# Performance work log

Measured on AMD Instinct MI355X. Metric: run time of the kernel, lower is better.

Reference implementation:

```python
import jax, jax.numpy as jnp
import numpy as np

N_SPARSE = 2  # keep N of every M weights (2:4 structured sparsity)
M_SPARSE = 4


def compute_mask(w, n, m):
    # w: [out, in]; zero the (m - n) smallest-|w| entries in each group of m
    out_f, in_f = w.shape
    k = m - n
    wr = jnp.abs(w).reshape(out_f, in_f // m, m)
    # indices of the k smallest |w| per group (torch.topk largest=False)
    _, idx = jax.lax.top_k(-wr, k)                      # [out, in/m, k]
    pruned = jax.nn.one_hot(idx, m, dtype=w.dtype).sum(axis=-2)  # [out, in/m, m]
    mask = 1.0 - pruned
    return mask.reshape(out_f, in_f)


def setup_inputs() -> dict:
    key = jax.random.key(0)
    k1, k2, k3 = jax.random.split(key, 3)
    B, S, Din, Dout = 64, 197, 768, 3072
    x = jax.random.normal(k1, (B, S, Din), dtype=jnp.float32)
    weight = jax.random.normal(k2, (Dout, Din), dtype=jnp.float32)
    bias = jax.random.normal(k3, (Dout,), dtype=jnp.float32)
    return {"x": x, "weight": weight, "bias": bias}


def reference(x, weight, bias):
    # mask is a precomputed buffer in torch (not differentiated)
    mask = compute_mask(jax.lax.stop_gradient(weight), N_SPARSE, M_SPARSE)
    w = weight * mask
    # F.linear: x @ w.T + b
    return jnp.einsum('bsi,oi->bso', x, w) + bias
```

## Files before the change

kernel.cpp:

```cpp
#include <hip/hip_runtime.h>
#include <hip/hip_bf16.h>

#define M_DIM 12608
#define K_DIM 768
#define N_DIM 3072
#define M_PAD 12800
#define BM 256
#define BN 128
#define BK 32

typedef __attribute__((ext_vector_type(8))) short bf16x8;
typedef __attribute__((ext_vector_type(4))) float f32x4;

__device__ __forceinline__ void gload_lds16(const void* g, void* l) {
  __builtin_amdgcn_global_load_lds(
      (const __attribute__((address_space(1))) unsigned int*)g,
      (__attribute__((address_space(3))) unsigned int*)l,
      16, 0, 0);
}

#define GX 4800
#define GW 2304
__global__ void cvt_fused(const float* __restrict__ x, const float* __restrict__ w,
                          __hip_bfloat16* __restrict__ xb, __hip_bfloat16* __restrict__ wb) {
  if (blockIdx.x < GX) {
    size_t i = ((size_t)blockIdx.x * 256 + threadIdx.x) * 8;
    union { __hip_bfloat16 h[8]; uint4 u; } o;
    if (i < (size_t)M_DIM * K_DIM) {
      float4 a = *(const float4*)(x + i);
      float4 b = *(const float4*)(x + i + 4);
      o.h[0] = __float2bfloat16(a.x); o.h[1] = __float2bfloat16(a.y);
      o.h[2] = __float2bfloat16(a.z); o.h[3] = __float2bfloat16(a.w);
      o.h[4] = __float2bfloat16(b.x); o.h[5] = __float2bfloat16(b.y);
      o.h[6] = __float2bfloat16(b.z); o.h[7] = __float2bfloat16(b.w);
    } else {
      o.u = make_uint4(0, 0, 0, 0);
    }
    *(uint4*)(xb + i) = o.u;
  } else {
    size_t g = ((size_t)(blockIdx.x - GX) * 256 + threadIdx.x);
    float4 v = *(const float4*)(w + g * 4);
    float val[4] = {v.x, v.y, v.z, v.w};
    float a[4] = {fabsf(v.x), fabsf(v.y), fabsf(v.z), fabsf(v.w)};
    union { __hip_bfloat16 h[4]; uint2 u; } o;
#pragma unroll
    for (int i = 0; i < 4; ++i) {
      int rank = 0;
#pragma unroll
      for (int j = 0; j < 4; ++j)
        rank += (a[j] > a[i]) || (a[j] == a[i] && j > i);
      o.h[i] = __float2bfloat16(rank < 2 ? val[i] : 0.0f);
    }
    *(uint2*)(wb + g * 4) = o.u;
  }
}

__global__ __launch_bounds__(256, 2) void gemm_bt(
    const __hip_bfloat16* __restrict__ A,
    const __hip_bfloat16* __restrict__ B,
    const float* __restrict__ bias,
    float* __restrict__ C)
{
  __shared__ char smem[49152];

  const int tid  = threadIdx.x;
  const int lane = tid & 63;
  const int wave = tid >> 6;

  const int tile_m = blockIdx.y * BM;
  const int tile_n = blockIdx.x * BN;

  const int ris  = lane >> 2;
  const int slot = lane & 3;
  const __hip_bfloat16* agp[4];
  const __hip_bfloat16* bgp[2];
#pragma unroll
  for (int i = 0; i < 4; ++i) {
    const int arow = wave * 64 + i * 16 + ris;
    const int acg = slot ^ (arow & 3) ^ ((arow >> 2) & 3);
    agp[i] = A + (size_t)(tile_m + arow) * K_DIM + acg * 8;
  }
#pragma unroll
  for (int i = 0; i < 2; ++i) {
    const int brow = wave * 32 + i * 16 + ris;
    const int bcg = slot ^ (brow & 3) ^ ((brow >> 2) & 3);
    bgp[i] = B + (size_t)(tile_n + brow) * K_DIM + bcg * 8;
  }

  const int frow  = lane & 15;
  const int fslot = (lane >> 4) ^ (frow & 3) ^ ((frow >> 2) & 3);

  f32x4 acc[4][8] = {};

#pragma unroll
  for (int i = 0; i < 4; ++i)
    gload_lds16(agp[i], smem + (wave * 4 + i) * 1024);
#pragma unroll
  for (int i = 0; i < 2; ++i)
    gload_lds16(bgp[i], smem + 16384 + (wave * 2 + i) * 1024);

  const int NITER = K_DIM / BK;
#pragma unroll 2
  for (int k = 0; k < NITER; ++k) {
    const int cur = k & 1;
    __syncthreads();

    if (k + 1 < NITER) {
      const int off = (k + 1) * BK;
      char* bb = smem + (cur ^ 1) * 24576;
#pragma unroll
      for (int i = 0; i < 4; ++i)
        gload_lds16(agp[i] + off, bb + (wave * 4 + i) * 1024);
#pragma unroll
      for (int i = 0; i < 2; ++i)
        gload_lds16(bgp[i] + off, bb + 16384 + (wave * 2 + i) * 1024);
    }

    const char* sa = smem + cur * 24576;
    bf16x8 af[4], bfr[8];
#pragma unroll
    for (int i = 0; i < 4; ++i)
      af[i] = *(const bf16x8*)(sa + (wave * 64 + i * 16 + frow) * 64 + fslot * 16);
#pragma unroll
    for (int j = 0; j < 8; ++j)
      bfr[j] = *(const bf16x8*)(sa + 16384 + (j * 16 + frow) * 64 + fslot * 16);
#pragma unroll
    for (int i = 0; i < 4; ++i)
#pragma unroll
      for (int j = 0; j < 8; ++j)
        acc[i][j] = __builtin_amdgcn_mfma_f32_16x16x32_bf16(af[i], bfr[j], acc[i][j], 0, 0, 0);
  }

  const int ccol = lane & 15;
  const int quad = lane >> 4;
  float bv[8];
#pragma unroll
  for (int j = 0; j < 8; ++j)
    bv[j] = bias[tile_n + j * 16 + ccol];

  float* tr = (float*)smem + wave * 2112;
  const int erow = lane >> 2;
  const int eseg = lane & 3;

#pragma unroll
  for (int i = 0; i < 4; ++i) {
    __syncthreads();
#pragma unroll
    for (int j = 0; j < 8; ++j)
#pragma unroll
      for (int r = 0; r < 4; ++r)
        tr[(quad * 4 + r) * 132 + j * 16 + ccol] = acc[i][j][r] + bv[j];
    __syncthreads();
    const int grow = tile_m + wave * 64 + i * 16 + erow;
    if (grow < M_DIM) {
      float* dst = C + (size_t)grow * N_DIM + tile_n + eseg * 32;
      const float* src = tr + erow * 132 + eseg * 32;
#pragma unroll
      for (int u = 0; u < 8; ++u)
        *(f32x4*)(dst + u * 4) = *(const f32x4*)(src + u * 4);
    }
  }
}

extern "C" void kernel_launch(void* const* d_in, const int* in_sizes, int n_in,
                              void* d_out, int out_size, void* d_ws, size_t ws_size,
                              hipStream_t stream) {
  const float* x    = (const float*)d_in[0];
  const float* w    = (const float*)d_in[1];
  const float* bias = (const float*)d_in[2];
  float* out = (float*)d_out;

  __hip_bfloat16* xb = (__hip_bfloat16*)d_ws;
  __hip_bfloat16* wb = xb + (size_t)M_PAD * K_DIM;

  cvt_fused<<<GX + GW, 256, 0, stream>>>(x, w, xb, wb);

  dim3 grid(N_DIM / BN, M_PAD / BM);
  gemm_bt<<<grid, 256, 0, stream>>>(xb, wb, bias, out);
}
```

Measured before the change: 269.1 us.

## Restructure GEMM to 256x256 tiles with 8 waves and 4-stage LDS pipeline

Replaces the 256x128, 4-wave GEMM with a 256x256 tile run by 8 waves arranged 2x4. It uses a 4-deep LDS ring of 32 KB stages held in 128 KB of dynamic shared memory and issues loads two tiles ahead with explicit vmcnt waits and raw barriers. Each K-step is split into two MFMA phases raised with s_setprio, and blocks are remapped through an XCD-aware swizzle. The goal is more reuse per loaded byte and better overlap of loads with compute, at the cost of higher register and LDS pressure, which may limit occupancy to one block per CU.

```diff
diff --git a/kernel.cpp b/kernel.cpp
--- a/kernel.cpp
+++ b/kernel.cpp
@@ -6,8 +6,12 @@
 #define N_DIM 3072
 #define M_PAD 12800
 #define BM 256
-#define BN 128
+#define BN 256
 #define BK 32
+#define NT (K_DIM / BK)
+#define MBLK (M_PAD / BM)
+#define NBLK_N (N_DIM / BN)
+#define NWG (MBLK * NBLK_N)
 
 typedef __attribute__((ext_vector_type(8))) short bf16x8;
 typedef __attribute__((ext_vector_type(4))) float f32x4;
@@ -55,109 +59,134 @@
   }
 }
 
-__global__ __launch_bounds__(256, 2) void gemm_bt(
+__global__ __launch_bounds__(512, 2) void gemm_8p(
     const __hip_bfloat16* __restrict__ A,
     const __hip_bfloat16* __restrict__ B,
     const float* __restrict__ bias,
     float* __restrict__ C)
 {
-  __shared__ char smem[49152];
+  extern __shared__ char smem[];
 
   const int tid  = threadIdx.x;
   const int lane = tid & 63;
   const int wave = tid >> 6;
-
-  const int tile_m = blockIdx.y * BM;
-  const int tile_n = blockIdx.x * BN;
-
-  const int ris  = lane >> 2;
-  const int slot = lane & 3;
-  const __hip_bfloat16* agp[4];
-  const __hip_bfloat16* bgp[2];
-#pragma unroll
-  for (int i = 0; i < 4; ++i) {
-    const int arow = wave * 64 + i * 16 + ris;
-    const int acg = slot ^ (arow & 3) ^ ((arow >> 2) & 3);
-    agp[i] = A + (size_t)(tile_m + arow) * K_DIM + acg * 8;
-  }
-#pragma unroll
-  for (int i = 0; i < 2; ++i) {
-    const int brow = wave * 32 + i * 16 + ris;
-    const int bcg = slot ^ (brow & 3) ^ ((brow >> 2) & 3);
-    bgp[i] = B + (size_t)(tile_n + brow) * K_DIM + bcg * 8;
+  const int wm   = wave >> 2;
+  const int wn   = wave & 3;
+
+  const int wg  = blockIdx.x;
+  const int swz = (wg & 7) * (NWG / 8) + (wg >> 3);
+  const int tile_m = (swz / NBLK_N) * BM;
+  const int tile_n = (swz % NBLK_N) * BN;
+
+  const int r2 = lane >> 2;
+  const int p  = lane & 3;
+  const int fxor = (r2 & 3) ^ ((r2 >> 2) & 3);
+  const int gsw  = p ^ fxor;
+  const __hip_bfloat16* asrc[2];
+  const __hip_bfloat16* bsrc[2];
+#pragma unroll
+  for (int u = 0; u < 2; ++u) {
+    const int row = u * 128 + wave * 16 + r2;
+    asrc[u] = A + (size_t)(tile_m + row) * K_DIM + gsw * 8;
+    bsrc[u] = B + (size_t)(tile_n + row) * K_DIM + gsw * 8;
   }
 
   const int frow  = lane & 15;
   const int fslot = (lane >> 4) ^ (frow & 3) ^ ((frow >> 2) & 3);
-
-  f32x4 acc[4][8] = {};
-
-#pragma unroll
-  for (int i = 0; i < 4; ++i)
-    gload_lds16(agp[i], smem + (wave * 4 + i) * 1024);
-#pragma unroll
-  for (int i = 0; i < 2; ++i)
-    gload_lds16(bgp[i], smem + 16384 + (wave * 2 + i) * 1024);
-
-  const int NITER = K_DIM / BK;
-#pragma unroll 2
-  for (int k = 0; k < NITER; ++k) {
-    const int cur = k & 1;
-    __syncthreads();
-
-    if (k + 1 < NITER) {
-      const int off = (k + 1) * BK;
-      char* bb = smem + (cur ^ 1) * 24576;
-#pragma unroll
-      for (int i = 0; i < 4; ++i)
-        gload_lds16(agp[i] + off, bb + (wave * 4 + i) * 1024);
-#pragma unroll
-      for (int i = 0; i < 2; ++i)
-        gload_lds16(bgp[i] + off, bb + 16384 + (wave * 2 + i) * 1024);
-    }
-
-    const char* sa = smem + cur * 24576;
-    bf16x8 af[4], bfr[8];
-#pragma unroll
-    for (int i = 0; i < 4; ++i)
-      af[i] = *(const bf16x8*)(sa + (wave * 64 + i * 16 + frow) * 64 + fslot * 16);
-#pragma unroll
-    for (int j = 0; j < 8; ++j)
-      bfr[j] = *(const bf16x8*)(sa + 16384 + (j * 16 + frow) * 64 + fslot * 16);
-#pragma unroll
-    for (int i = 0; i < 4; ++i)
-#pragma unroll
-      for (int j = 0; j < 8; ++j)
-        acc[i][j] = __builtin_amdgcn_mfma_f32_16x16x32_bf16(af[i], bfr[j], acc[i][j], 0, 0, 0);
+  const int abase = (wm * 128 + frow) * 64 + fslot * 16;
+  const int bbase = 16384 + (wn * 64 + frow) * 64 + fslot * 16;
+
+  f32x4 acc[8][4] = {};
+
+#pragma unroll
+  for (int u = 0; u < 2; ++u)
+    gload_lds16(asrc[u], smem + u * 8192 + wave * 1024);
+#pragma unroll
+  for (int u = 0; u < 2; ++u)
+    gload_lds16(bsrc[u], smem + 16384 + u * 8192 + wave * 1024);
+#pragma unroll
+  for (int u = 0; u < 2; ++u)
+    gload_lds16(asrc[u] + BK, smem + 32768 + u * 8192 + wave * 1024);
+#pragma unroll
+  for (int u = 0; u < 2; ++u)
+    gload_lds16(bsrc[u] + BK, smem + 32768 + 16384 + u * 8192 + wave * 1024);
+  asm volatile("s_waitcnt vmcnt(4)" ::: "memory");
+  __builtin_amdgcn_s_barrier();
+
+#pragma unroll
+  for (int t = 0; t < NT; ++t) {
+    const int q  = t & 3;
+    const int qs = (t + 2) & 3;
+    const char* bq = smem + q * 32768;
+
+    bf16x8 af[4], bfv[4];
+#pragma unroll
+    for (int m = 0; m < 4; ++m)
+      af[m] = *(const bf16x8*)(bq + abase + m * 1024);
+#pragma unroll
+    for (int n = 0; n < 4; ++n)
+      bfv[n] = *(const bf16x8*)(bq + bbase + n * 1024);
+    if (t + 2 < NT) {
+#pragma unroll
+      for (int u = 0; u < 2; ++u)
+        gload_lds16(asrc[u] + (t + 2) * BK, smem + qs * 32768 + u * 8192 + wave * 1024);
+    }
+    __builtin_amdgcn_s_barrier();
+    __builtin_amdgcn_s_setprio(1);
+#pragma unroll
+    for (int m = 0; m < 4; ++m)
+#pragma unroll
+      for (int n = 0; n < 4; ++n)
+        acc[m][n] = __builtin_amdgcn_mfma_f32_16x16x32_bf16(af[m], bfv[n], acc[m][n], 0, 0, 0);
+    __builtin_amdgcn_s_setprio(0);
+    __builtin_amdgcn_s_barrier();
+
+    bf16x8 af2[4];
+#pragma unroll
+    for (int m = 0; m < 4; ++m)
+      af2[m] = *(const bf16x8*)(bq + abase + (4 + m) * 1024);
+    if (t + 2 < NT) {
+#pragma unroll
+      for (int u = 0; u < 2; ++u)
+        gload_lds16(bsrc[u] + (t + 2) * BK, smem + qs * 32768 + 16384 + u * 8192 + wave * 1024);
+    }
+    if (t < NT - 2)       { asm volatile("s_waitcnt vmcnt(4)" ::: "memory"); }
+    else if (t == NT - 2) { asm volatile("s_waitcnt vmcnt(0)" ::: "memory"); }
+    __builtin_amdgcn_s_barrier();
+    __builtin_amdgcn_s_setprio(1);
+#pragma unroll
+    for (int m = 0; m < 4; ++m)
+#pragma unroll
+      for (int n = 0; n < 4; ++n)
+        acc[4 + m][n] = __builtin_amdgcn_mfma_f32_16x16x32_bf16(af2[m], bfv[n], acc[4 + m][n], 0, 0, 0);
+    __builtin_amdgcn_s_setprio(0);
+    __builtin_amdgcn_s_barrier();
   }
 
   const int ccol = lane & 15;
   const int quad = lane >> 4;
-  float bv[8];
-#pragma unroll
-  for (int j = 0; j < 8; ++j)
-    bv[j] = bias[tile_n + j * 16 + ccol];
-
-  float* tr = (float*)smem + wave * 2112;
+  float bv[4];
+#pragma unroll
+  for (int n = 0; n < 4; ++n)
+    bv[n] = bias[tile_n + wn * 64 + n * 16 + ccol];
+
+  float* tr = (float*)smem + wave * 1088;
   const int erow = lane >> 2;
-  const int eseg = lane & 3;
-
-#pragma unroll
-  for (int i = 0; i < 4; ++i) {
-    __syncthreads();
-#pragma unroll
-    for (int j = 0; j < 8; ++j)
+  const int es   = lane & 3;
+
+#pragma unroll
+  for (int m = 0; m < 8; ++m) {
+#pragma unroll
+    for (int n = 0; n < 4; ++n)
 #pragma unroll
       for (int r = 0; r < 4; ++r)
-        tr[(quad * 4 + r) * 132 + j * 16 + ccol] = acc[i][j][r] + bv[j];
-    __syncthreads();
-    const int grow = tile_m + wave * 64 + i * 16 + erow;
+        tr[(quad * 4 + r) * 68 + n * 16 + ccol] = acc[m][n][r] + bv[n];
+    const int grow = tile_m + wm * 128 + m * 16 + erow;
     if (grow < M_DIM) {
-      float* dst = C + (size_t)grow * N_DIM + tile_n + eseg * 32;
-      const float* src = tr + erow * 132 + eseg * 32;
-#pragma unroll
-      for (int u = 0; u < 8; ++u)
-        *(f32x4*)(dst + u * 4) = *(const f32x4*)(src + u * 4);
+      float* dst = C + (size_t)grow * N_DIM + tile_n + wn * 64;
+#pragma unroll
+      for (int u = 0; u < 4; ++u)
+        *(f32x4*)(dst + u * 16 + es * 4) = *(const f32x4*)(tr + erow * 68 + u * 16 + es * 4);
     }
   }
 }
@@ -173,8 +202,13 @@
   __hip_bfloat16* xb = (__hip_bfloat16*)d_ws;
   __hip_bfloat16* wb = xb + (size_t)M_PAD * K_DIM;
 
+  static bool attr_set = false;
+  if (!attr_set) {
+    hipFuncSetAttribute(reinterpret_cast<const void*>(gemm_8p),
+                        hipFuncAttributeMaxDynamicSharedMemorySize, 131072);
+    attr_set = true;
+  }
+
   cvt_fused<<<GX + GW, 256, 0, stream>>>(x, w, xb, wb);
-
-  dim3 grid(N_DIM / BN, M_PAD / BM);
-  gemm_bt<<<grid, 256, 0, stream>>>(xb, wb, bias, out);
-}
+  gemm_8p<<<NWG, 512, 131072, stream>>>(xb, wb, bias, out);
+}
```

Measured after the change: 248.3 us. 7.7% less time.
